# Kernel tuning notes

Hardware: AMD Instinct MI355X
Metric: run time of the kernel (lower is better)

Reference implementation:

```python
import jax, jax.numpy as jnp
import numpy as np

N_NODES = 100000
N_EDGES = 800000
F_IN = 128
HID = 128
HEADS = 4
HEAD_DIM = HID // HEADS
LAYERS = 3
N_CLASSES = 40
NEG_SLOPE = 0.2
BN_EPS = 1e-5


def setup_inputs() -> dict:
    key = jax.random.key(0)
    ks = jax.random.split(key, 10)
    feat = jax.random.normal(ks[0], (N_NODES, F_IN), dtype=jnp.float32)
    src = jax.random.randint(ks[1], (N_EDGES,), 0, N_NODES, dtype=jnp.int32)
    dst = jax.random.randint(ks[2], (N_EDGES,), 0, N_NODES, dtype=jnp.int32)
    W_enc = jax.random.normal(ks[3], (F_IN, HID), dtype=jnp.float32) / np.sqrt(F_IN)
    b_enc = jnp.zeros((HID,), dtype=jnp.float32)
    Ws = jax.random.normal(ks[4], (LAYERS, HID, HID), dtype=jnp.float32) / np.sqrt(HID)
    attn_ls = jax.random.normal(ks[5], (LAYERS, HEADS, HEAD_DIM), dtype=jnp.float32) / np.sqrt(HEAD_DIM)
    attn_rs = jax.random.normal(ks[6], (LAYERS, HEADS, HEAD_DIM), dtype=jnp.float32) / np.sqrt(HEAD_DIM)
    biases = jnp.zeros((LAYERS, HID), dtype=jnp.float32)
    gammas = jnp.ones((LAYERS, HID), dtype=jnp.float32)
    betas = jnp.zeros((LAYERS, HID), dtype=jnp.float32)
    W_pred = jax.random.normal(ks[7], (HID, N_CLASSES), dtype=jnp.float32) / np.sqrt(HID)
    b_pred = jnp.zeros((N_CLASSES,), dtype=jnp.float32)
    return {"feat": feat, "src": src, "dst": dst, "W_enc": W_enc, "b_enc": b_enc,
            "Ws": Ws, "attn_ls": attn_ls, "attn_rs": attn_rs, "biases": biases,
            "gammas": gammas, "betas": betas, "W_pred": W_pred, "b_pred": b_pred}


def _gat_layer(h, src, dst, W, a_l, a_r, bias, n_nodes):
    # h: [N, HID] -> projected per-head features [N, H, D]
    hf = (h @ W).reshape(n_nodes, HEADS, HEAD_DIM)
    el = jnp.sum(hf * a_l, axis=-1)  # [N, H]
    er = jnp.sum(hf * a_r, axis=-1)  # [N, H]
    e = jax.nn.leaky_relu(el[src] + er[dst], NEG_SLOPE)  # [E, H]
    # edge softmax over incoming edges of each destination node
    m = jax.ops.segment_max(e, dst, num_segments=n_nodes)  # [N, H]
    ex = jnp.exp(e - m[dst])
    s = jax.ops.segment_sum(ex, dst, num_segments=n_nodes)  # [N, H]
    alpha = ex / s[dst]  # [E, H]
    msg = hf[src] * alpha[:, :, None]  # [E, H, D]
    out = jax.ops.segment_sum(msg, dst, num_segments=n_nodes)  # [N, H, D]
    return out.reshape(n_nodes, HEADS * HEAD_DIM) + bias


def _batchnorm(x, gamma, beta):
    mean = jnp.mean(x, axis=0)
    var = jnp.var(x, axis=0)
    return gamma * (x - mean) * jax.lax.rsqrt(var + BN_EPS) + beta


def reference(feat, src, dst, W_enc, b_enc, Ws, attn_ls, attn_rs, biases, gammas, betas, W_pred, b_pred):
    n_nodes = feat.shape[0]
    h = jax.nn.relu(feat @ W_enc + b_enc)
    h_last = None
    for i in range(Ws.shape[0]):
        h = _gat_layer(h, src, dst, Ws[i], attn_ls[i], attn_rs[i], biases[i], n_nodes)
        if h_last is not None:
            h = h + h_last
        h_last = h
        h = _batchnorm(h, gammas[i], betas[i])
        h = jax.nn.relu(h)
    return h @ W_pred + b_pred
```

## Files before the change

kernel.cpp:

```cpp
#include <hip/hip_runtime.h>

typedef __attribute__((ext_vector_type(8))) short short8;
typedef __attribute__((ext_vector_type(4))) float f32x4;

#define N_NODES 100000
#define N_EDGES 800000
#define NEG 0.2f
#define BN_EPS 1e-5f
#define AGG_GRID 2048
#define MG_GRID 1024
#define MG_TILES 3125

__device__ __forceinline__ ushort bf16b(float f) {
  unsigned u = __float_as_uint(f);
  return (ushort)((u + 0x7FFFu + ((u >> 16) & 1u)) >> 16);
}
__device__ __forceinline__ float bflo(unsigned u) { return __uint_as_float(u << 16); }
__device__ __forceinline__ float bfhi(unsigned u) { return __uint_as_float(u & 0xFFFF0000u); }

__global__ void k_hist(const int* __restrict__ dst, int* __restrict__ cnt, int e) {
  int i = blockIdx.x * blockDim.x + threadIdx.x;
  if (i < e) atomicAdd(&cnt[dst[i]], 1);
}

__global__ void k_scan1(const int* __restrict__ cnt, int* __restrict__ rowptr,
                        int* __restrict__ bsums, int n) {
  __shared__ int sm[256];
  int i = blockIdx.x * 256 + threadIdx.x;
  int v = (i < n) ? cnt[i] : 0;
  sm[threadIdx.x] = v;
  __syncthreads();
  for (int off = 1; off < 256; off <<= 1) {
    int t = (threadIdx.x >= off) ? sm[threadIdx.x - off] : 0;
    __syncthreads();
    sm[threadIdx.x] += t;
    __syncthreads();
  }
  if (i < n) rowptr[i + 1] = sm[threadIdx.x];
  if (threadIdx.x == 255) bsums[blockIdx.x] = sm[255];
}

__global__ void k_scan2(int* __restrict__ bsums, int nb) {
  __shared__ int sm[512];
  int v = (threadIdx.x < nb) ? bsums[threadIdx.x] : 0;
  sm[threadIdx.x] = v;
  __syncthreads();
  for (int off = 1; off < 512; off <<= 1) {
    int t = (threadIdx.x >= off) ? sm[threadIdx.x - off] : 0;
    __syncthreads();
    sm[threadIdx.x] += t;
    __syncthreads();
  }
  if (threadIdx.x < nb) bsums[threadIdx.x] = sm[threadIdx.x] - v;
}

__global__ void k_scan3(int* __restrict__ rowptr, const int* __restrict__ bsums,
                        int* __restrict__ cursor, int n) {
  int i = blockIdx.x * 256 + threadIdx.x;
  if (i < n) {
    int val = rowptr[i + 1] + bsums[blockIdx.x];
    rowptr[i + 1] = val;
    if (i + 1 < n) cursor[i + 1] = val;
  }
  if (i == 0) { rowptr[0] = 0; cursor[0] = 0; }
}

__global__ void k_scatter(const int* __restrict__ src, const int* __restrict__ dst,
                          int* __restrict__ cursor, int2* __restrict__ esort, int e) {
  int i = blockIdx.x * blockDim.x + threadIdx.x;
  if (i < e) {
    int d = dst[i];
    int pos = atomicAdd(&cursor[d], 1);
    long long packed = (long long)(((unsigned long long)(unsigned)d << 32) |
                                   (unsigned long long)(unsigned)src[i]);
    __builtin_nontemporal_store(packed, (long long*)&esort[pos]);
  }
}

__global__ void k_packW(const float* __restrict__ W_enc, const float* __restrict__ Ws,
                        ushort* __restrict__ Wp) {
  int s = blockIdx.x * 256 + threadIdx.x;
  int wi = s >> 11, s2 = s & 2047;
  int kt = s2 >> 9, nb8 = (s2 >> 6) & 7, l = s2 & 63;
  const float* Wsrc = (wi == 0) ? W_enc : Ws + (size_t)(wi - 1) * 16384;
  int n = nb8 * 16 + (l & 15);
  int k0 = kt * 32 + (l >> 4) * 8;
  unsigned pk[4];
#pragma unroll
  for (int j = 0; j < 4; ++j) {
    ushort lo = bf16b(Wsrc[(size_t)(k0 + 2 * j) * 128 + n]);
    ushort hi = bf16b(Wsrc[(size_t)(k0 + 2 * j + 1) * 128 + n]);
    pk[j] = (unsigned)lo | ((unsigned)hi << 16);
  }
  *(uint4*)&Wp[(size_t)s * 8] = make_uint4(pk[0], pk[1], pk[2], pk[3]);
}

template <int MODE>
__global__ __launch_bounds__(256) void k_mgemm(
    const float* __restrict__ Af, const ushort* __restrict__ Ab,
    const ushort* __restrict__ Wp, const float* __restrict__ bias,
    const float* __restrict__ stats, const float* __restrict__ al,
    const float* __restrict__ ar, float* __restrict__ el, float* __restrict__ er,
    float4* __restrict__ blockmax, ushort* __restrict__ Cb) {
  __shared__ __align__(16) ushort Al[32 * 128];
  int tid = threadIdx.x;
  int lane = tid & 63, w = tid >> 6;
  int wr = w & 1, wc = w >> 1;
  int l15 = lane & 15, l4 = lane >> 4;

  const uint4* wp4 = (const uint4*)Wp;
  short8 bfr[4][4];
#pragma unroll
  for (int kt = 0; kt < 4; ++kt) {
#pragma unroll
    for (int nb = 0; nb < 4; ++nb) {
      uint4 t = wp4[(size_t)((kt * 8 + wc * 4 + nb) * 64 + lane)];
      bfr[kt][nb] = *(short8*)&t;
    }
  }

  float alv0 = 0, alv1 = 0, alv2 = 0, alv3 = 0;
  float arv0 = 0, arv1 = 0, arv2 = 0, arv3 = 0;
  float bv0 = 0, bv1 = 0, bv2 = 0, bv3 = 0;
  if (MODE != 0) {
    alv0 = al[64 * wc + l15];      arv0 = ar[64 * wc + l15];
    alv1 = al[64 * wc + 16 + l15]; arv1 = ar[64 * wc + 16 + l15];
    alv2 = al[64 * wc + 32 + l15]; arv2 = ar[64 * wc + 32 + l15];
    alv3 = al[64 * wc + 48 + l15]; arv3 = ar[64 * wc + 48 + l15];
  } else {
    bv0 = bias[64 * wc + l15];      bv1 = bias[64 * wc + 16 + l15];
    bv2 = bias[64 * wc + 32 + l15]; bv3 = bias[64 * wc + 48 + l15];
  }

  float gmx0 = -1e30f, gmx1 = -1e30f;

  int srow = tid >> 3;
  int c16 = (tid & 7) * 16;
  int kc0 = (tid & 7) * 2;
  int arow = 16 * wr + l15;
  const char* abase = (const char*)Al + arow * 256;
  int sw = arow & 7;

  for (int tile = blockIdx.x; tile < MG_TILES; tile += MG_GRID) {
    int rb = tile * 32;
    __syncthreads();
    {
      char* base = (char*)Al + srow * 256;
      if (MODE == 1) {
        const uint4* srcp = (const uint4*)(Ab + (size_t)(rb + srow) * 128 + c16);
        uint4 v0 = srcp[0], v1 = srcp[1];
        *(uint4*)(base + ((kc0 ^ (srow & 7)) << 4)) = v0;
        *(uint4*)(base + (((kc0 + 1) ^ (srow & 7)) << 4)) = v1;
      } else if (MODE == 2) {
        const uint4* srcp = (const uint4*)(Ab + (size_t)(rb + srow) * 128 + c16);
        uint4 v0 = srcp[0], v1 = srcp[1];
        unsigned pk[8];
#pragma unroll
        for (int j = 0; j < 4; ++j) {
          unsigned wv = ((const unsigned*)&v0)[j];
          float2 sc = *(const float2*)&stats[c16 + 2 * j];
          float2 sh = *(const float2*)&stats[128 + c16 + 2 * j];
          float x0 = fmaxf(bflo(wv) * sc.x + sh.x, 0.f);
          float x1 = fmaxf(bfhi(wv) * sc.y + sh.y, 0.f);
          pk[j] = (unsigned)bf16b(x0) | ((unsigned)bf16b(x1) << 16);
        }
#pragma unroll
        for (int j = 0; j < 4; ++j) {
          unsigned wv = ((const unsigned*)&v1)[j];
          float2 sc = *(const float2*)&stats[c16 + 8 + 2 * j];
          float2 sh = *(const float2*)&stats[128 + c16 + 8 + 2 * j];
          float x0 = fmaxf(bflo(wv) * sc.x + sh.x, 0.f);
          float x1 = fmaxf(bfhi(wv) * sc.y + sh.y, 0.f);
          pk[4 + j] = (unsigned)bf16b(x0) | ((unsigned)bf16b(x1) << 16);
        }
        *(uint4*)(base + ((kc0 ^ (srow & 7)) << 4)) = make_uint4(pk[0], pk[1], pk[2], pk[3]);
        *(uint4*)(base + (((kc0 + 1) ^ (srow & 7)) << 4)) = make_uint4(pk[4], pk[5], pk[6], pk[7]);
      } else {
        const float4* srcp = (const float4*)(Af + (size_t)(rb + srow) * 128 + c16);
        float4 f[4];
#pragma unroll
        for (int j = 0; j < 4; ++j) f[j] = srcp[j];
        unsigned pk[8];
#pragma unroll
        for (int j = 0; j < 4; ++j) {
          pk[2 * j] = (unsigned)bf16b(f[j].x) | ((unsigned)bf16b(f[j].y) << 16);
          pk[2 * j + 1] = (unsigned)bf16b(f[j].z) | ((unsigned)bf16b(f[j].w) << 16);
        }
        *(uint4*)(base + ((kc0 ^ (srow & 7)) << 4)) = make_uint4(pk[0], pk[1], pk[2], pk[3]);
        *(uint4*)(base + (((kc0 + 1) ^ (srow & 7)) << 4)) = make_uint4(pk[4], pk[5], pk[6], pk[7]);
      }
    }
    __syncthreads();

    f32x4 acc[4];
#pragma unroll
    for (int nb = 0; nb < 4; ++nb) acc[nb] = (f32x4){0.f, 0.f, 0.f, 0.f};
#pragma unroll
    for (int kt = 0; kt < 4; ++kt) {
      short8 af = *(const short8*)(abase + (((kt * 4 + l4) ^ sw) << 4));
      acc[0] = __builtin_amdgcn_mfma_f32_16x16x32_bf16(af, bfr[kt][0], acc[0], 0, 0, 0);
      acc[1] = __builtin_amdgcn_mfma_f32_16x16x32_bf16(af, bfr[kt][1], acc[1], 0, 0, 0);
      acc[2] = __builtin_amdgcn_mfma_f32_16x16x32_bf16(af, bfr[kt][2], acc[2], 0, 0, 0);
      acc[3] = __builtin_amdgcn_mfma_f32_16x16x32_bf16(af, bfr[kt][3], acc[3], 0, 0, 0);
    }

    int row0 = rb + 16 * wr + 4 * l4;
#pragma unroll
    for (int i = 0; i < 4; ++i) {
      int row = row0 + i;
      if (MODE != 0) {
        float pl0 = acc[0][i] * alv0 + acc[1][i] * alv1;
        float pr0 = acc[0][i] * arv0 + acc[1][i] * arv1;
        float pl1 = acc[2][i] * alv2 + acc[3][i] * alv3;
        float pr1 = acc[2][i] * arv2 + acc[3][i] * arv3;
#pragma unroll
        for (int o = 1; o < 16; o <<= 1) {
          pl0 += __shfl_xor(pl0, o); pr0 += __shfl_xor(pr0, o);
          pl1 += __shfl_xor(pl1, o); pr1 += __shfl_xor(pr1, o);
        }
        gmx0 = fmaxf(gmx0, pl0); gmx1 = fmaxf(gmx1, pl1);
        if (l15 == 0) {
          el[(size_t)row * 4 + 2 * wc] = pl0;     er[(size_t)row * 4 + 2 * wc] = pr0;
          el[(size_t)row * 4 + 2 * wc + 1] = pl1; er[(size_t)row * 4 + 2 * wc + 1] = pr1;
        }
      }
      float v0 = acc[0][i], v1 = acc[1][i], v2 = acc[2][i], v3 = acc[3][i];
      if (MODE == 0) {
        v0 = fmaxf(v0 + bv0, 0.f); v1 = fmaxf(v1 + bv1, 0.f);
        v2 = fmaxf(v2 + bv2, 0.f); v3 = fmaxf(v3 + bv3, 0.f);
      }
      size_t rbase = (size_t)row * 128 + 64 * wc + l15;
      Cb[rbase] = bf16b(v0);
      Cb[rbase + 16] = bf16b(v1);
      Cb[rbase + 32] = bf16b(v2);
      Cb[rbase + 48] = bf16b(v3);
    }
  }

  if (MODE != 0) {
    gmx0 = fmaxf(gmx0, __shfl_xor(gmx0, 16)); gmx0 = fmaxf(gmx0, __shfl_xor(gmx0, 32));
    gmx1 = fmaxf(gmx1, __shfl_xor(gmx1, 16)); gmx1 = fmaxf(gmx1, __shfl_xor(gmx1, 32));
    __shared__ float lm[4][2];
    if (lane == 0) { lm[w][0] = gmx0; lm[w][1] = gmx1; }
    __syncthreads();
    if (tid == 0) {
      float4 bm;
      bm.x = fmaxf(lm[0][0], lm[1][0]);
      bm.y = fmaxf(lm[0][1], lm[1][1]);
      bm.z = fmaxf(lm[2][0], lm[3][0]);
      bm.w = fmaxf(lm[2][1], lm[3][1]);
      blockmax[blockIdx.x] = bm;
    }
  }
}

__global__ __launch_bounds__(256) void k_elmax2(const float4* __restrict__ bm,
                                                float* __restrict__ elmax, int g) {
  float4 m = make_float4(-1e30f, -1e30f, -1e30f, -1e30f);
  for (int i = threadIdx.x; i < g; i += 256) {
    float4 v = bm[i];
    m.x = fmaxf(m.x, v.x); m.y = fmaxf(m.y, v.y);
    m.z = fmaxf(m.z, v.z); m.w = fmaxf(m.w, v.w);
  }
  __shared__ float4 sm[256];
  sm[threadIdx.x] = m;
  __syncthreads();
  for (int off = 128; off; off >>= 1) {
    if (threadIdx.x < off) {
      float4 o = sm[threadIdx.x + off];
      sm[threadIdx.x].x = fmaxf(sm[threadIdx.x].x, o.x);
      sm[threadIdx.x].y = fmaxf(sm[threadIdx.x].y, o.y);
      sm[threadIdx.x].z = fmaxf(sm[threadIdx.x].z, o.z);
      sm[threadIdx.x].w = fmaxf(sm[threadIdx.x].w, o.w);
    }
    __syncthreads();
  }
  if (threadIdx.x == 0) {
    elmax[0] = sm[0].x; elmax[1] = sm[0].y;
    elmax[2] = sm[0].z; elmax[3] = sm[0].w;
  }
}

__global__ __launch_bounds__(256) void k_edgew(
    const int2* __restrict__ esort, const float* __restrict__ el,
    const float* __restrict__ er, const float* __restrict__ elmax,
    float4* __restrict__ wgt, int e) {
  int j = blockIdx.x * 256 + threadIdx.x;
  if (j >= e) return;
  int2 sd = esort[j];
  float4 elv = *(const float4*)&el[(size_t)4 * sd.x];
  float4 erv = *(const float4*)&er[(size_t)4 * sd.y];
  float m0 = elmax[0] + erv.x;
  float m1 = elmax[1] + erv.y;
  float m2 = elmax[2] + erv.z;
  float m3 = elmax[3] + erv.w;
  m0 = fmaxf(m0, NEG * m0); m1 = fmaxf(m1, NEG * m1);
  m2 = fmaxf(m2, NEG * m2); m3 = fmaxf(m3, NEG * m3);
  float e0 = elv.x + erv.x; e0 = fmaxf(e0, NEG * e0);
  float e1 = elv.y + erv.y; e1 = fmaxf(e1, NEG * e1);
  float e2 = elv.z + erv.z; e2 = fmaxf(e2, NEG * e2);
  float e3 = elv.w + erv.w; e3 = fmaxf(e3, NEG * e3);
  float4 wv;
  wv.x = __expf(e0 - m0); wv.y = __expf(e1 - m1);
  wv.z = __expf(e2 - m2); wv.w = __expf(e3 - m3);
  wgt[j] = wv;
}

__global__ __launch_bounds__(256, 8) void k_aggregate(
    const ushort* __restrict__ hf, const float4* __restrict__ wgt,
    const int* __restrict__ rowptr, const int2* __restrict__ esort,
    const float* __restrict__ bias, ushort* __restrict__ hpre,
    float* __restrict__ part, int n, int addres) {
  int tid = threadIdx.x;
  int w = tid >> 6, lane = tid & 63;
  int h = lane >> 4;
  int c0 = 2 * lane;
  float2 bb = *(const float2*)&bias[c0];
  float sbn0 = 0.f, sbn1 = 0.f, qbn0 = 0.f, qbn1 = 0.f;
  for (int wid = blockIdx.x * 4 + w; wid < n; wid += AGG_GRID * 4) {
    int beg = rowptr[wid], end = rowptr[wid + 1];
    float s0 = 0.f, a00 = 0.f, a10 = 0.f;
    float s1 = 0.f, a01 = 0.f, a11 = 0.f;
    float s2 = 0.f, a02 = 0.f, a12 = 0.f;
    float s3 = 0.f, a03 = 0.f, a13 = 0.f;
    int j = beg;
    int rem = (end - beg) & 3;
    for (int t = 0; t < rem; ++t, ++j) {
      int sA = esort[j].x;
      float wA = ((const float*)(wgt + j))[h];
      unsigned hA = *(const unsigned*)(hf + (size_t)sA * 128 + c0);
      s0 += wA; a00 += wA * bflo(hA); a10 += wA * bfhi(hA);
    }
    for (; j < end; j += 4) {
      int sA = esort[j].x, sB = esort[j + 1].x, sC = esort[j + 2].x, sD = esort[j + 3].x;
      float wA = ((const float*)(wgt + j))[h];
      float wB = ((const float*)(wgt + j + 1))[h];
      float wC = ((const float*)(wgt + j + 2))[h];
      float wD = ((const float*)(wgt + j + 3))[h];
      unsigned hA = *(const unsigned*)(hf + (size_t)sA * 128 + c0);
      unsigned hB = *(const unsigned*)(hf + (size_t)sB * 128 + c0);
      unsigned hC = *(const unsigned*)(hf + (size_t)sC * 128 + c0);
      unsigned hD = *(const unsigned*)(hf + (size_t)sD * 128 + c0);
      s0 += wA; a00 += wA * bflo(hA); a10 += wA * bfhi(hA);
      s1 += wB; a01 += wB * bflo(hB); a11 += wB * bfhi(hB);
      s2 += wC; a02 += wC * bflo(hC); a12 += wC * bfhi(hC);
      s3 += wD; a03 += wD * bflo(hD); a13 += wD * bfhi(hD);
    }
    float s = (s0 + s1) + (s2 + s3);
    float inv = (end > beg) ? 1.f / s : 0.f;
    float a0 = ((a00 + a01) + (a02 + a03)) * inv;
    float a1 = ((a10 + a11) + (a12 + a13)) * inv;
    float r0 = 0.f, r1 = 0.f;
    if (addres) {
      unsigned rr = *(const unsigned*)(hpre + (size_t)wid * 128 + c0);
      r0 = bflo(rr); r1 = bfhi(rr);
    }
    float o0 = a0 + bb.x + r0, o1 = a1 + bb.y + r1;
    *(unsigned*)(hpre + (size_t)wid * 128 + c0) =
        (unsigned)bf16b(o0) | ((unsigned)bf16b(o1) << 16);
    sbn0 += o0; qbn0 += o0 * o0;
    sbn1 += o1; qbn1 += o1 * o1;
  }
  __shared__ float red_s[4][128];
  __shared__ float red_q[4][128];
  red_s[w][c0] = sbn0; red_s[w][c0 + 1] = sbn1;
  red_q[w][c0] = qbn0; red_q[w][c0 + 1] = qbn1;
  __syncthreads();
  if (tid < 128)
    part[(size_t)blockIdx.x * 256 + tid] =
        (red_s[0][tid] + red_s[1][tid]) + (red_s[2][tid] + red_s[3][tid]);
  else if (tid < 256) {
    int c = tid - 128;
    part[(size_t)blockIdx.x * 256 + tid] =
        (red_q[0][c] + red_q[1][c]) + (red_q[2][c] + red_q[3][c]);
  }
}

__global__ __launch_bounds__(320) void k_pred(
    const ushort* __restrict__ A, const float* __restrict__ stats,
    const float* __restrict__ W, const float* __restrict__ bias,
    float* __restrict__ out, int n) {
  __shared__ float Wl[128 * 40];
  __shared__ float Xl[32 * 132];
  for (int i = threadIdx.x; i < 128 * 40; i += 320) Wl[i] = W[i];
  int cg = threadIdx.x % 10;
  int rg = threadIdx.x / 10;
  float4 bv = *(const float4*)&bias[4 * cg];
  for (int rb = blockIdx.x * 32; rb < n; rb += gridDim.x * 32) {
    __syncthreads();
    for (int idx = threadIdx.x; idx < 1024; idx += 320) {
      int r = idx >> 5, c = (idx & 31) * 4;
      uint2 v = *(const uint2*)(A + (size_t)(rb + r) * 128 + c);
      float4 sc = *(const float4*)&stats[c];
      float4 sh = *(const float4*)&stats[128 + c];
      float x0 = fmaxf(bflo(v.x) * sc.x + sh.x, 0.f);
      float x1 = fmaxf(bfhi(v.x) * sc.y + sh.y, 0.f);
      float x2 = fmaxf(bflo(v.y) * sc.z + sh.z, 0.f);
      float x3 = fmaxf(bfhi(v.y) * sc.w + sh.w, 0.f);
      *(float4*)&Xl[r * 132 + c] = make_float4(x0, x1, x2, x3);
    }
    __syncthreads();
    float a0 = 0.f, a1 = 0.f, a2 = 0.f, a3 = 0.f;
#pragma unroll 4
    for (int k = 0; k < 128; ++k) {
      float x = Xl[rg * 132 + k];
      float4 w = *(float4*)&Wl[k * 40 + 4 * cg];
      a0 += x * w.x; a1 += x * w.y; a2 += x * w.z; a3 += x * w.w;
    }
    float4 o = make_float4(a0 + bv.x, a1 + bv.y, a2 + bv.z, a3 + bv.w);
    *(float4*)&out[(size_t)(rb + rg) * 40 + 4 * cg] = o;
  }
}

__global__ __launch_bounds__(256) void k_bnred(
    const float* __restrict__ part, float* __restrict__ colsum,
    const float* __restrict__ gamma, const float* __restrict__ beta,
    float* __restrict__ stats, unsigned* __restrict__ ctr, int g, int n) {
  int v = blockIdx.x;
  float acc = 0.f;
  for (int b = threadIdx.x; b < g; b += 256) acc += part[(size_t)b * 256 + v];
  __shared__ float sm[256];
  sm[threadIdx.x] = acc;
  __syncthreads();
  for (int off = 128; off; off >>= 1) {
    if (threadIdx.x < off) sm[threadIdx.x] += sm[threadIdx.x + off];
    __syncthreads();
  }
  __shared__ int last;
  if (threadIdx.x == 0) {
    colsum[v] = sm[0];
    __threadfence();
    last = (atomicAdd(ctr, 1u) == (unsigned)(gridDim.x - 1));
  }
  __syncthreads();
  if (last) {
    __threadfence();
    if (threadIdx.x == 0) *ctr = 0;
    if (threadIdx.x < 128) {
      int c = threadIdx.x;
      float mean = colsum[c] / n;
      float var = colsum[128 + c] / n - mean * mean;
      float rstd = rsqrtf(var + BN_EPS);
      float scale = gamma[c] * rstd;
      stats[c] = scale;
      stats[128 + c] = beta[c] - mean * scale;
    }
  }
}

extern "C" void kernel_launch(void* const* d_in, const int* in_sizes, int n_in,
                              void* d_out, int out_size, void* d_ws, size_t ws_size,
                              hipStream_t stream) {
  const float* feat   = (const float*)d_in[0];
  const int*   src    = (const int*)d_in[1];
  const int*   dst    = (const int*)d_in[2];
  const float* W_enc  = (const float*)d_in[3];
  const float* b_enc  = (const float*)d_in[4];
  const float* Ws     = (const float*)d_in[5];
  const float* a_ls   = (const float*)d_in[6];
  const float* a_rs   = (const float*)d_in[7];
  const float* biases = (const float*)d_in[8];
  const float* gammas = (const float*)d_in[9];
  const float* betas  = (const float*)d_in[10];
  const float* W_pred = (const float*)d_in[11];
  const float* b_pred = (const float*)d_in[12];
  float* out = (float*)d_out;

  char* p = (char*)d_ws;
  auto alloc = [&](size_t bytes) {
    char* q = p;
    p += (bytes + 255) & ~(size_t)255;
    return q;
  };
  ushort* h_bf  = (ushort*)alloc((size_t)N_NODES * 128 * 2);
  ushort* hf_bf = (ushort*)alloc((size_t)N_NODES * 128 * 2);
  ushort* hpre  = (ushort*)alloc((size_t)N_NODES * 128 * 2);
  float* el     = (float*)alloc((size_t)N_NODES * 4 * 4);
  float* er     = (float*)alloc((size_t)N_NODES * 4 * 4);
  float* part   = (float*)alloc((size_t)AGG_GRID * 256 * 4);
  float* colsum = (float*)alloc(256 * 4);
  float* stats  = (float*)alloc(256 * 4);
  ushort* Wpack = (ushort*)alloc((size_t)4 * 2048 * 16);
  float4* bmax  = (float4*)alloc((size_t)MG_GRID * 16);
  float* elmax  = (float*)alloc(4 * 4);
  unsigned* ctr = (unsigned*)alloc(256);
  int* rowptr   = (int*)alloc((size_t)(N_NODES + 1) * 4);
  int* cursor   = (int*)alloc((size_t)N_NODES * 4);
  int* bsums    = (int*)alloc(512 * 4);
  int2* esort   = (int2*)alloc((size_t)N_EDGES * 8);
  float4* wgt   = (float4*)alloc((size_t)N_EDGES * 16);

  hipMemsetAsync(cursor, 0, (size_t)N_NODES * 4, stream);
  hipMemsetAsync(ctr, 0, 4, stream);
  k_hist<<<(N_EDGES + 255) / 256, 256, 0, stream>>>(dst, cursor, N_EDGES);
  int nb = (N_NODES + 255) / 256;
  k_scan1<<<nb, 256, 0, stream>>>(cursor, rowptr, bsums, N_NODES);
  k_scan2<<<1, 512, 0, stream>>>(bsums, nb);
  k_scan3<<<nb, 256, 0, stream>>>(rowptr, bsums, cursor, N_NODES);
  k_scatter<<<(N_EDGES + 255) / 256, 256, 0, stream>>>(src, dst, cursor, esort, N_EDGES);

  k_packW<<<32, 256, 0, stream>>>(W_enc, Ws, Wpack);

  k_mgemm<0><<<MG_GRID, 256, 0, stream>>>(feat, nullptr, Wpack, b_enc, nullptr, nullptr,
                                          nullptr, nullptr, nullptr, nullptr, h_bf);

  for (int L = 0; L < 3; ++L) {
    const float* al = a_ls + L * 128;
    const float* ar = a_rs + L * 128;
    const ushort* wp = Wpack + (size_t)(1 + L) * 16384;
    if (L == 0)
      k_mgemm<1><<<MG_GRID, 256, 0, stream>>>(nullptr, h_bf, wp, nullptr, nullptr, al,
                                              ar, el, er, bmax, hf_bf);
    else
      k_mgemm<2><<<MG_GRID, 256, 0, stream>>>(nullptr, hpre, wp, nullptr, stats, al,
                                              ar, el, er, bmax, hf_bf);
    k_elmax2<<<1, 256, 0, stream>>>(bmax, elmax, MG_GRID);
    k_edgew<<<(N_EDGES + 255) / 256, 256, 0, stream>>>(esort, el, er, elmax, wgt,
                                                       N_EDGES);
    k_aggregate<<<AGG_GRID, 256, 0, stream>>>(hf_bf, wgt, rowptr, esort,
                                              biases + L * 128, hpre, part, N_NODES,
                                              L > 0 ? 1 : 0);
    k_bnred<<<256, 256, 0, stream>>>(part, colsum, gammas + L * 128, betas + L * 128,
                                     stats, ctr, AGG_GRID, N_NODES);
  }
  k_pred<<<1563, 320, 0, stream>>>(hpre, stats, W_pred, b_pred, out, N_NODES);
}
```

Measured before the change: 439.9 us.

## Fuse elmax reduction into GEMM via last-block pattern and pad aggregate tail

```diff
diff --git a/kernel.cpp b/kernel.cpp
--- a/kernel.cpp
+++ b/kernel.cpp
@@ -71,9 +71,7 @@
   if (i < e) {
     int d = dst[i];
     int pos = atomicAdd(&cursor[d], 1);
-    long long packed = (long long)(((unsigned long long)(unsigned)d << 32) |
-                                   (unsigned long long)(unsigned)src[i]);
-    __builtin_nontemporal_store(packed, (long long*)&esort[pos]);
+    esort[pos] = make_int2(src[i], d);
   }
 }
 
@@ -101,7 +99,8 @@
     const ushort* __restrict__ Wp, const float* __restrict__ bias,
     const float* __restrict__ stats, const float* __restrict__ al,
     const float* __restrict__ ar, float* __restrict__ el, float* __restrict__ er,
-    float4* __restrict__ blockmax, ushort* __restrict__ Cb) {
+    float4* __restrict__ blockmax, float* __restrict__ elmax,
+    unsigned* __restrict__ mctr, ushort* __restrict__ Cb) {
   __shared__ __align__(16) ushort Al[32 * 128];
   int tid = threadIdx.x;
   int lane = tid & 63, w = tid >> 6;
@@ -243,6 +242,7 @@
     __shared__ float lm[4][2];
     if (lane == 0) { lm[w][0] = gmx0; lm[w][1] = gmx1; }
     __syncthreads();
+    __shared__ int lastf;
     if (tid == 0) {
       float4 bm;
       bm.x = fmaxf(lm[0][0], lm[1][0]);
@@ -250,34 +250,37 @@
       bm.z = fmaxf(lm[2][0], lm[3][0]);
       bm.w = fmaxf(lm[2][1], lm[3][1]);
       blockmax[blockIdx.x] = bm;
-    }
-  }
-}
-
-__global__ __launch_bounds__(256) void k_elmax2(const float4* __restrict__ bm,
-                                                float* __restrict__ elmax, int g) {
-  float4 m = make_float4(-1e30f, -1e30f, -1e30f, -1e30f);
-  for (int i = threadIdx.x; i < g; i += 256) {
-    float4 v = bm[i];
-    m.x = fmaxf(m.x, v.x); m.y = fmaxf(m.y, v.y);
-    m.z = fmaxf(m.z, v.z); m.w = fmaxf(m.w, v.w);
-  }
-  __shared__ float4 sm[256];
-  sm[threadIdx.x] = m;
-  __syncthreads();
-  for (int off = 128; off; off >>= 1) {
-    if (threadIdx.x < off) {
-      float4 o = sm[threadIdx.x + off];
-      sm[threadIdx.x].x = fmaxf(sm[threadIdx.x].x, o.x);
-      sm[threadIdx.x].y = fmaxf(sm[threadIdx.x].y, o.y);
-      sm[threadIdx.x].z = fmaxf(sm[threadIdx.x].z, o.z);
-      sm[threadIdx.x].w = fmaxf(sm[threadIdx.x].w, o.w);
-    }
-    __syncthreads();
-  }
-  if (threadIdx.x == 0) {
-    elmax[0] = sm[0].x; elmax[1] = sm[0].y;
-    elmax[2] = sm[0].z; elmax[3] = sm[0].w;
+      __threadfence();
+      lastf = (atomicAdd(mctr, 1u) == (unsigned)(MG_GRID - 1));
+    }
+    __syncthreads();
+    if (lastf) {
+      __threadfence();
+      float4 m = make_float4(-1e30f, -1e30f, -1e30f, -1e30f);
+      for (int i = tid; i < MG_GRID; i += 256) {
+        float4 v = blockmax[i];
+        m.x = fmaxf(m.x, v.x); m.y = fmaxf(m.y, v.y);
+        m.z = fmaxf(m.z, v.z); m.w = fmaxf(m.w, v.w);
+      }
+      __shared__ float4 smx[256];
+      smx[tid] = m;
+      __syncthreads();
+      for (int off = 128; off; off >>= 1) {
+        if (tid < off) {
+          float4 o = smx[tid + off];
+          smx[tid].x = fmaxf(smx[tid].x, o.x);
+          smx[tid].y = fmaxf(smx[tid].y, o.y);
+          smx[tid].z = fmaxf(smx[tid].z, o.z);
+          smx[tid].w = fmaxf(smx[tid].w, o.w);
+        }
+        __syncthreads();
+      }
+      if (tid == 0) {
+        elmax[0] = smx[0].x; elmax[1] = smx[0].y;
+        elmax[2] = smx[0].z; elmax[3] = smx[0].w;
+        *mctr = 0;
+      }
+    }
   }
 }
 
@@ -324,19 +327,30 @@
     float s2 = 0.f, a02 = 0.f, a12 = 0.f;
     float s3 = 0.f, a03 = 0.f, a13 = 0.f;
     int j = beg;
-    int rem = (end - beg) & 3;
-    for (int t = 0; t < rem; ++t, ++j) {
-      int sA = esort[j].x;
-      float wA = ((const float*)(wgt + j))[h];
-      unsigned hA = *(const unsigned*)(hf + (size_t)sA * 128 + c0);
-      s0 += wA; a00 += wA * bflo(hA); a10 += wA * bfhi(hA);
-    }
-    for (; j < end; j += 4) {
+    for (; j + 4 <= end; j += 4) {
       int sA = esort[j].x, sB = esort[j + 1].x, sC = esort[j + 2].x, sD = esort[j + 3].x;
       float wA = ((const float*)(wgt + j))[h];
       float wB = ((const float*)(wgt + j + 1))[h];
       float wC = ((const float*)(wgt + j + 2))[h];
       float wD = ((const float*)(wgt + j + 3))[h];
+      unsigned hA = *(const unsigned*)(hf + (size_t)sA * 128 + c0);
+      unsigned hB = *(const unsigned*)(hf + (size_t)sB * 128 + c0);
+      unsigned hC = *(const unsigned*)(hf + (size_t)sC * 128 + c0);
+      unsigned hD = *(const unsigned*)(hf + (size_t)sD * 128 + c0);
+      s0 += wA; a00 += wA * bflo(hA); a10 += wA * bfhi(hA);
+      s1 += wB; a01 += wB * bflo(hB); a11 += wB * bfhi(hB);
+      s2 += wC; a02 += wC * bflo(hC); a12 += wC * bfhi(hC);
+      s3 += wD; a03 += wD * bflo(hD); a13 += wD * bfhi(hD);
+    }
+    if (j < end) {
+      int jB = (j + 1 < end) ? j + 1 : j;
+      int jC = (j + 2 < end) ? j + 2 : j;
+      int jD = (j + 3 < end) ? j + 3 : j;
+      int sA = esort[j].x, sB = esort[jB].x, sC = esort[jC].x, sD = esort[jD].x;
+      float wA = ((const float*)(wgt + j))[h];
+      float wB = (j + 1 < end) ? ((const float*)(wgt + jB))[h] : 0.f;
+      float wC = (j + 2 < end) ? ((const float*)(wgt + jC))[h] : 0.f;
+      float wD = (j + 3 < end) ? ((const float*)(wgt + jD))[h] : 0.f;
       unsigned hA = *(const unsigned*)(hf + (size_t)sA * 128 + c0);
       unsigned hB = *(const unsigned*)(hf + (size_t)sB * 128 + c0);
       unsigned hC = *(const unsigned*)(hf + (size_t)sC * 128 + c0);
@@ -491,7 +505,7 @@
   float4* wgt   = (float4*)alloc((size_t)N_EDGES * 16);
 
   hipMemsetAsync(cursor, 0, (size_t)N_NODES * 4, stream);
-  hipMemsetAsync(ctr, 0, 4, stream);
+  hipMemsetAsync(ctr, 0, 8, stream);
   k_hist<<<(N_EDGES + 255) / 256, 256, 0, stream>>>(dst, cursor, N_EDGES);
   int nb = (N_NODES + 255) / 256;
   k_scan1<<<nb, 256, 0, stream>>>(cursor, rowptr, bsums, N_NODES);
@@ -502,7 +516,8 @@
   k_packW<<<32, 256, 0, stream>>>(W_enc, Ws, Wpack);
 
   k_mgemm<0><<<MG_GRID, 256, 0, stream>>>(feat, nullptr, Wpack, b_enc, nullptr, nullptr,
-                                          nullptr, nullptr, nullptr, nullptr, h_bf);
+                                          nullptr, nullptr, nullptr, nullptr, nullptr,
+                                          nullptr, h_bf);
 
   for (int L = 0; L < 3; ++L) {
     const float* al = a_ls + L * 128;
@@ -510,11 +525,10 @@
     const ushort* wp = Wpack + (size_t)(1 + L) * 16384;
     if (L == 0)
       k_mgemm<1><<<MG_GRID, 256, 0, stream>>>(nullptr, h_bf, wp, nullptr, nullptr, al,
-                                              ar, el, er, bmax, hf_bf);
+                                              ar, el, er, bmax, elmax, ctr + 1, hf_bf);
     else
       k_mgemm<2><<<MG_GRID, 256, 0, stream>>>(nullptr, hpre, wp, nullptr, stats, al,
-                                              ar, el, er, bmax, hf_bf);
-    k_elmax2<<<1, 256, 0, stream>>>(bmax, elmax, MG_GRID);
+                                              ar, el, er, bmax, elmax, ctr + 1, hf_bf);
     k_edgew<<<(N_EDGES + 255) / 256, 256, 0, stream>>>(esort, el, er, elmax, wgt,
                                                        N_EDGES);
     k_aggregate<<<AGG_GRID, 256, 0, stream>>>(hf_bf, wgt, rowptr, esort,
```

Result: slower. 531.3 us (+20.8%).
